# Optimization experiments

Hardware: AMD Instinct MI355X
Metric: run time of the kernel (lower is better)

The kernel has to match this reference:

```python
import jax, jax.numpy as jnp
import numpy as np

B, S, D = 2, 2048, 2048
H, Dh = 16, 128  # qkv_features = H*Dh = 2048
NEG = -1e10


def setup_inputs() -> dict:
    key = jax.random.key(0)
    k1, k2, k3 = jax.random.split(key, 3)
    x = jax.random.normal(k1, (B, S, D), dtype=jnp.float32)
    # variance_scaling(1.0, 'fan_in', 'normal') ~ std = 1/sqrt(fan_in)
    Wqkv = jax.random.normal(k2, (D, 3 * H * Dh), dtype=jnp.float32) / np.sqrt(D)
    bqkv = jnp.zeros((3 * H * Dh,), dtype=jnp.float32)
    Wout = jax.random.normal(k3, (H * Dh, D), dtype=jnp.float32) / np.sqrt(H * Dh)
    bout = jnp.zeros((D,), dtype=jnp.float32)
    return {"x": x, "Wqkv": Wqkv, "bqkv": bqkv, "Wout": Wout, "bout": bout}


def reference(x, Wqkv, bqkv, Wout, bout):
    b, s, _ = x.shape
    # fused QKV projection
    qkv = x @ Wqkv + bqkv                                   # [B, S, 3*H*Dh]
    qkv = qkv.reshape(b, s, 3, H, Dh).transpose(2, 0, 3, 1, 4)  # [3, B, H, S, Dh]
    q, k, v = qkv[0], qkv[1], qkv[2]
    scale = 1.0 / jnp.sqrt(jnp.asarray(Dh, dtype=x.dtype))
    # Each query chunk attends to the full key sequence with a causal mask,
    # which is mathematically full causal attention.
    scores = jnp.einsum('bhqd,bhkd->bhqk', q, k) * scale    # [B, H, S, S]
    causal = jnp.arange(s)[None, :] <= jnp.arange(s)[:, None]  # k <= q
    scores = jnp.where(causal[None, None, :, :], scores, NEG)
    weights = jax.nn.softmax(scores, axis=-1)
    out = jnp.einsum('bhqk,bhkd->bhqd', weights, v)         # [B, H, S, Dh]
    out = out.transpose(0, 2, 1, 3).reshape(b, s, H * Dh)
    return out @ Wout + bout
```

## Files before the change

### kernel.cpp

```cpp
#include <hip/hip_runtime.h>


typedef unsigned short u16;
typedef __attribute__((ext_vector_type(8))) short bf16x8;
typedef __attribute__((ext_vector_type(4))) float f32x4;

#define MFMA(a, b, c) __builtin_amdgcn_mfma_f32_16x16x32_bf16((a), (b), (c), 0, 0, 0)

__device__ __forceinline__ u16 f2bf(float f) {
    unsigned u = __builtin_bit_cast(unsigned, f);
    u += 0x7fffu + ((u >> 16) & 1u);
    return (u16)(u >> 16);
}

__device__ __forceinline__ void gload16(const void* g, void* l) {
    __builtin_amdgcn_global_load_lds(
        (const __attribute__((address_space(1))) void*)g,
        (__attribute__((address_space(3))) void*)l, 16, 0, 0);
}


__global__ __launch_bounds__(256) void k_cast(const float* __restrict__ src,
                                              u16* __restrict__ dst, int n4) {
    int i = blockIdx.x * 256 + threadIdx.x;
    if (i >= n4) return;
    float4 a = ((const float4*)src)[i];
    ushort4 r;
    r.x = f2bf(a.x); r.y = f2bf(a.y); r.z = f2bf(a.z); r.w = f2bf(a.w);
    ((ushort4*)dst)[i] = r;
}

__global__ __launch_bounds__(256) void k_castT(const float* __restrict__ src,
                                               u16* __restrict__ dst, int rows, int cols) {
    __shared__ float t[32][33];
    int c0 = blockIdx.x * 32, r0 = blockIdx.y * 32;
    int tx = threadIdx.x, ty = threadIdx.y;
#pragma unroll
    for (int i = 0; i < 4; ++i)
        t[ty + 8 * i][tx] = src[(size_t)(r0 + ty + 8 * i) * cols + (c0 + tx)];
    __syncthreads();
#pragma unroll
    for (int i = 0; i < 4; ++i)
        dst[(size_t)(c0 + ty + 8 * i) * rows + (r0 + tx)] = f2bf(t[tx][ty + 8 * i]);
}

__global__ __launch_bounds__(256) void k_transv(const u16* __restrict__ v,
                                                u16* __restrict__ vT) {
    __shared__ u16 t[32][33];
    int head = blockIdx.z;
    int s0 = blockIdx.x * 32, d0 = blockIdx.y * 32;
    const u16* vp = v + (size_t)head * 2048 * 128;
    u16* op = vT + (size_t)head * 128 * 2048;
    int tx = threadIdx.x, ty = threadIdx.y;
#pragma unroll
    for (int i = 0; i < 4; ++i)
        t[ty + 8 * i][tx] = vp[(size_t)(s0 + ty + 8 * i) * 128 + d0 + tx];
    __syncthreads();
#pragma unroll
    for (int i = 0; i < 4; ++i)
        op[(size_t)(d0 + 8 * i + ty) * 2048 + (s0 + tx)] = t[tx][ty + 8 * i];
}


template <int K>
__device__ __forceinline__ void gemm_core64(const u16* __restrict__ A,
                                            const u16* __restrict__ BT,
                                            int m0, int n0,
                                            f32x4 (&acc)[4][4],
                                            u16* As, u16* Bs) {
    const int tid = threadIdx.x, wave = tid >> 6, lane = tid & 63;
    const int wr = (wave >> 1) * 64, wc = (wave & 1) * 64;
    char* AsB = (char*)As;
    char* BsB = (char*)Bs;
    for (int k0 = 0; k0 < K; k0 += 64) {
        __syncthreads();
#pragma unroll
        for (int i = 0; i < 4; ++i) {
            int cb = (i * 4 + wave) * 64;
            int d = (cb + lane) * 16;
            int row = d >> 7;
            int co = (d & 127) ^ ((row & 7) << 4);
            gload16(A + (size_t)(m0 + row) * K + k0 + (co >> 1), AsB + cb * 16);
            gload16(BT + (size_t)(n0 + row) * K + k0 + (co >> 1), BsB + cb * 16);
        }
        __syncthreads();
        bf16x8 a[2][4], b[2][4];
#pragma unroll
        for (int ks = 0; ks < 2; ++ks)
#pragma unroll
            for (int m = 0; m < 4; ++m) {
                int row = wr + m * 16 + (lane & 15);
                a[ks][m] = *(const bf16x8*)(AsB +
                    ((row * 128 + ks * 64 + (lane >> 4) * 16) ^ ((row & 7) << 4)));
            }
#pragma unroll
        for (int ks = 0; ks < 2; ++ks)
#pragma unroll
            for (int n = 0; n < 4; ++n) {
                int row = wc + n * 16 + (lane & 15);
                b[ks][n] = *(const bf16x8*)(BsB +
                    ((row * 128 + ks * 64 + (lane >> 4) * 16) ^ ((row & 7) << 4)));
            }
        __builtin_amdgcn_s_setprio(1);
#pragma unroll
        for (int ks = 0; ks < 2; ++ks)
#pragma unroll
            for (int m = 0; m < 4; ++m)
#pragma unroll
                for (int n = 0; n < 4; ++n)
                    acc[m][n] = MFMA(a[ks][m], b[ks][n], acc[m][n]);
        __builtin_amdgcn_s_setprio(0);
    }
}

__global__ __launch_bounds__(256) void k_gemm_qkv(const u16* __restrict__ A,
                                                  const u16* __restrict__ BT,
                                                  const float* __restrict__ bias,
                                                  u16* __restrict__ q,
                                                  u16* __restrict__ kbuf,
                                                  u16* __restrict__ v) {
    __shared__ __align__(16) u16 As[128 * 64];
    __shared__ __align__(16) u16 Bs[128 * 64];
    f32x4 acc[4][4] = {};
    const int orig = blockIdx.y * 48 + blockIdx.x;
    const int xcd = orig & 7, idx = orig >> 3;
    const int n_blk = xcd * 6 + idx % 6, m_blk = idx / 6;
    const int m0 = m_blk * 128, n0 = n_blk * 128;
    gemm_core64<2048>(A, BT, m0, n0, acc, As, Bs);

    const int tid = threadIdx.x, wave = tid >> 6, lane = tid & 63;
    const int wr = (wave >> 1) * 64, wc = (wave & 1) * 64;
    const int t = n0 >> 11;
    u16* dst = (t == 0) ? q : (t == 1) ? kbuf : v;
#pragma unroll
    for (int m = 0; m < 4; ++m)
#pragma unroll
        for (int n = 0; n < 4; ++n)
#pragma unroll
            for (int j = 0; j < 4; ++j) {
                int gr = m0 + wr + m * 16 + (lane >> 4) * 4 + j;
                int gc = n0 + wc + n * 16 + (lane & 15);
                float val = acc[m][n][j] + bias[gc];
                int bb = gr >> 11, s = gr & 2047;
                int rem = gc & 2047, h = rem >> 7, d = rem & 127;
                dst[((size_t)(bb * 16 + h) * 2048 + s) * 128 + d] = f2bf(val);
            }
}

__global__ __launch_bounds__(256) void k_gemm_out(const u16* __restrict__ A,
                                                  const u16* __restrict__ BT,
                                                  const float* __restrict__ bias,
                                                  float* __restrict__ out) {
    __shared__ __align__(16) u16 As[128 * 64];
    __shared__ __align__(16) u16 Bs[128 * 64];
    f32x4 acc[4][4] = {};
    const int orig = blockIdx.y * 16 + blockIdx.x;
    const int nb = (orig & 7) * 64 + (orig >> 3);
    const int m0 = (nb / 16) * 128, n0 = (nb % 16) * 128;
    gemm_core64<2048>(A, BT, m0, n0, acc, As, Bs);

    const int tid = threadIdx.x, wave = tid >> 6, lane = tid & 63;
    const int wr = (wave >> 1) * 64, wc = (wave & 1) * 64;
#pragma unroll
    for (int m = 0; m < 4; ++m)
#pragma unroll
        for (int n = 0; n < 4; ++n)
#pragma unroll
            for (int j = 0; j < 4; ++j) {
                int gr = m0 + wr + m * 16 + (lane >> 4) * 4 + j;
                int gc = n0 + wc + n * 16 + (lane & 15);
                out[(size_t)gr * 2048 + gc] = acc[m][n][j] + bias[gc];
            }
}

__global__ __launch_bounds__(512) void k_attn(const u16* __restrict__ q,
                                              const u16* __restrict__ k,
                                              const u16* __restrict__ vT,
                                              u16* __restrict__ o) {
    __shared__ __align__(16) u16 KsA[2 * 64 * 128];
    __shared__ __align__(16) u16 VsA[2 * 128 * 64];
    __shared__ __align__(16) u16 PsA[8 * 16 * 64];
    char* ksB = (char*)KsA;
    char* vsB = (char*)VsA;

    const int tid = threadIdx.x, wave = tid >> 6, lane = tid & 63;
    char* psB = (char*)PsA + wave * 2048;

    const int lin = blockIdx.x;
    const int dd = (lin & 7) * 32 + (lin >> 3);
    const int head = dd >> 3, pair = dd & 7;

    const u16* qh = q + (size_t)head * 2048 * 128;
    const u16* kh = k + (size_t)head * 2048 * 128;
    const u16* vh = vT + (size_t)head * 128 * 2048;
    const int bb = head >> 4, hh = head & 15;
    const float qscale = 0.1275293562566334f;
    const float MFIX = 20.f;

    bf16x8 ones;
#pragma unroll
    for (int e = 0; e < 8; ++e) ones[e] = (short)0x3F80;

    auto stage = [&](int kv0, int bufsel) {
        char* kd = ksB + bufsel * 16384;
        char* vd = vsB + bufsel * 16384;
#pragma unroll
        for (int i = 0; i < 2; ++i) {
            int cb = (i * 8 + wave) * 64;
            int d = (cb + lane) * 16;
            int r = d >> 8;
            int co = (d & 255) ^ ((r & 7) << 4);
            gload16(kh + (size_t)(kv0 + r) * 128 + (co >> 1), kd + cb * 16);
        }
#pragma unroll
        for (int i = 0; i < 2; ++i) {
            int cb = (i * 8 + wave) * 64;
            int d = (cb + lane) * 16;
            int vr = d >> 7;
            int co = (d & 127) ^ ((vr & 7) << 4);
            gload16(vh + (size_t)vr * 2048 + kv0 + (co >> 1), vd + cb * 16);
        }
    };

#pragma unroll 1
    for (int qsel = 0; qsel < 2; ++qsel) {
        const int qi = qsel ? (15 - pair) : pair;
        const int q0 = qi * 128;
        const int ntile = 2 * qi + 2;

        bf16x8 qf[4];
        const int qr = q0 + wave * 16 + (lane & 15);
#pragma unroll
        for (int kt = 0; kt < 4; ++kt)
            qf[kt] = *(const bf16x8*)(qh + (size_t)qr * 128 + kt * 32 + (lane >> 4) * 8);

        f32x4 o_acc[8] = {};
        f32x4 l_r = {};

        stage(0, 0);
        int buf = 0;

#pragma unroll 1
        for (int t = 0; t < ntile; ++t) {
            const int kv0 = t * 64;
            if (t + 1 < ntile) {
                stage(kv0 + 64, buf ^ 1);
                asm volatile("s_waitcnt vmcnt(4)" ::: "memory");
            } else {
                asm volatile("s_waitcnt vmcnt(0)" ::: "memory");
            }
            __builtin_amdgcn_s_barrier();
            char* kb_ = ksB + buf * 16384;
            char* vb_ = vsB + buf * 16384;

            if (kv0 <= q0 + wave * 16 + 15) {
                f32x4 s_acc[4] = {};
                __builtin_amdgcn_s_setprio(1);
#pragma unroll
                for (int c = 0; c < 4; ++c) {
                    int row = c * 16 + (lane & 15);
#pragma unroll
                    for (int kt = 0; kt < 4; ++kt) {
                        bf16x8 kbf = *(const bf16x8*)(kb_ +
                            ((row * 256 + kt * 64 + (lane >> 4) * 16) ^ ((row & 7) << 4)));
                        s_acc[c] = MFMA(qf[kt], kbf, s_acc[c]);
                    }
                }
                __builtin_amdgcn_s_setprio(0);

                const bool maskblk = (kv0 + 64 > q0 + wave * 16);
#pragma unroll
                for (int j = 0; j < 4; ++j) {
                    int qg = q0 + wave * 16 + (lane >> 4) * 4 + j;
#pragma unroll
                    for (int c = 0; c < 4; ++c) {
                        float sv = fmaf(s_acc[c][j], qscale, -MFIX);
                        if (maskblk && (kv0 + c * 16 + (lane & 15)) > qg) sv = -1e30f;
                        s_acc[c][j] = exp2f(sv);
                    }
                }

#pragma unroll
                for (int c = 0; c < 4; ++c)
#pragma unroll
                    for (int j = 0; j < 4; ++j) {
                        int row = (lane >> 4) * 4 + j;
                        *(u16*)(psB + ((row * 128 + (c * 16 + (lane & 15)) * 2) ^ ((row & 7) << 4)))
                            = f2bf(s_acc[c][j]);
                    }
                bf16x8 pf[2];
#pragma unroll
                for (int kt = 0; kt < 2; ++kt) {
                    int row2 = lane & 15;
                    pf[kt] = *(const bf16x8*)(psB +
                        ((row2 * 128 + kt * 64 + (lane >> 4) * 16) ^ ((row2 & 7) << 4)));
                }

                __builtin_amdgcn_s_setprio(1);
                l_r = MFMA(pf[0], ones, l_r);
                l_r = MFMA(pf[1], ones, l_r);
#pragma unroll
                for (int c2 = 0; c2 < 8; ++c2) {
#pragma unroll
                    for (int kt = 0; kt < 2; ++kt) {
                        int row = c2 * 16 + (lane & 15);
                        bf16x8 vf = *(const bf16x8*)(vb_ +
                            ((row * 128 + kt * 64 + (lane >> 4) * 16) ^ ((row & 7) << 4)));
                        o_acc[c2] = MFMA(pf[kt], vf, o_acc[c2]);
                    }
                }
                __builtin_amdgcn_s_setprio(0);
            }

            __builtin_amdgcn_s_barrier();
            buf ^= 1;
        }

        float linv[4];
#pragma unroll
        for (int j = 0; j < 4; ++j) linv[j] = 1.0f / l_r[j];
#pragma unroll
        for (int c2 = 0; c2 < 8; ++c2)
#pragma unroll
            for (int j = 0; j < 4; ++j) {
                int qg = q0 + wave * 16 + (lane >> 4) * 4 + j;
                int d2 = c2 * 16 + (lane & 15);
                o[((size_t)(bb * 2048 + qg)) * 2048 + hh * 128 + d2]
                    = f2bf(o_acc[c2][j] * linv[j]);
            }
    }
}


extern "C" void kernel_launch(void* const* d_in, const int* in_sizes, int n_in,
                              void* d_out, int out_size, void* d_ws, size_t ws_size,
                              hipStream_t stream) {
    const float* x    = (const float*)d_in[0];
    const float* Wqkv = (const float*)d_in[1];
    const float* bqkv = (const float*)d_in[2];
    const float* Wout = (const float*)d_in[3];
    const float* bout = (const float*)d_in[4];
    float* out = (float*)d_out;

    char* ws = (char*)d_ws;
    const size_t SZ = 16777216;
    u16* q   = (u16*)(ws);
    u16* kb  = (u16*)(ws + SZ);
    u16* v   = (u16*)(ws + 2 * SZ);
    u16* vT  = (u16*)(ws + 3 * SZ);
    u16* ao  = v;
    u16* xb  = (u16*)(ws + 4 * SZ);
    u16* WqT = (u16*)(ws + 5 * SZ);
    u16* WoT = (u16*)(ws + 5 * SZ + 25165824);

    k_cast<<<dim3(8192), dim3(256), 0, stream>>>(x, xb, 2097152);
    k_castT<<<dim3(192, 64), dim3(32, 8), 0, stream>>>(Wqkv, WqT, 2048, 6144);
    k_castT<<<dim3(64, 64), dim3(32, 8), 0, stream>>>(Wout, WoT, 2048, 2048);
    k_gemm_qkv<<<dim3(48, 32), dim3(256), 0, stream>>>(xb, WqT, bqkv, q, kb, v);
    k_transv<<<dim3(64, 4, 32), dim3(32, 8), 0, stream>>>(v, vT);
    k_attn<<<dim3(256), dim3(512), 0, stream>>>(q, kb, vT, ao);
    k_gemm_out<<<dim3(16, 32), dim3(256), 0, stream>>>(ao, WoT, bout, out);
}
```

Baseline: 253.2 us.

## Split long causal query tiles across KV blocks and read V from global

The attention launch grows from 256 to 768 blocks. Each block handles one 128-row query tile and a range of KV tiles, driven by a packed lookup table. For the longer tiles (qi >= 8) the KV range is split in two; each half writes unnormalized fp32 partial outputs and row sums to workspace, and a new k_final kernel adds the halves, normalizes and writes bf16. V fragments are now read straight from global memory instead of being staged through LDS, which halves the async staging traffic and frees shared memory. The aim is better load balance and more parallelism across CUs. The cost is an extra kernel, extra fp32 traffic, and possibly less efficient uncoalesced global V reads.

```diff
diff --git a/kernel.cpp b/kernel.cpp
--- a/kernel.cpp
+++ b/kernel.cpp
@@ -2,6 +2,7 @@
 
 
 typedef unsigned short u16;
+typedef unsigned long long u64;
 typedef __attribute__((ext_vector_type(8))) short bf16x8;
 typedef __attribute__((ext_vector_type(4))) float f32x4;
 
@@ -176,19 +177,28 @@
 __global__ __launch_bounds__(512) void k_attn(const u16* __restrict__ q,
                                               const u16* __restrict__ k,
                                               const u16* __restrict__ vT,
-                                              u16* __restrict__ o) {
+                                              u16* __restrict__ o,
+                                              float* __restrict__ Opart,
+                                              float* __restrict__ Lpart) {
     __shared__ __align__(16) u16 KsA[2 * 64 * 128];
-    __shared__ __align__(16) u16 VsA[2 * 128 * 64];
     __shared__ __align__(16) u16 PsA[8 * 16 * 64];
     char* ksB = (char*)KsA;
-    char* vsB = (char*)VsA;
 
     const int tid = threadIdx.x, wave = tid >> 6, lane = tid & 63;
     char* psB = (char*)PsA + wave * 2048;
 
     const int lin = blockIdx.x;
-    const int dd = (lin & 7) * 32 + (lin >> 3);
-    const int head = dd >> 3, pair = dd & 7;
+    const int x = lin & 7, local = lin >> 3;
+    const int head = x * 4 + (local & 3);
+    const int e = local >> 2;
+    const u64 qiT0 = 0x9AA5BBCC6DDEE7FFull;
+    const u64 qiT1 = 0x0000000001238849ull;
+    const u64 ptT  = 0x0000AA4912449124ull;
+    const int qi   = (int)(((e < 16 ? (qiT0 >> (e * 4)) : (qiT1 >> ((e - 16) * 4)))) & 15);
+    const int part = (int)((ptT >> (2 * e)) & 3);
+    const int q0 = qi * 128;
+    const int t0 = (part == 1) ? (qi + 1) : 0;
+    const int t1 = (part == 0) ? (qi + 1) : (2 * qi + 2);
 
     const u16* qh = q + (size_t)head * 2048 * 128;
     const u16* kh = k + (size_t)head * 2048 * 128;
@@ -199,11 +209,10 @@
 
     bf16x8 ones;
 #pragma unroll
-    for (int e = 0; e < 8; ++e) ones[e] = (short)0x3F80;
-
-    auto stage = [&](int kv0, int bufsel) {
+    for (int ee = 0; ee < 8; ++ee) ones[ee] = (short)0x3F80;
+
+    auto stageK = [&](int kv0, int bufsel) {
         char* kd = ksB + bufsel * 16384;
-        char* vd = vsB + bufsel * 16384;
 #pragma unroll
         for (int i = 0; i < 2; ++i) {
             int cb = (i * 8 + wave) * 64;
@@ -212,110 +221,96 @@
             int co = (d & 255) ^ ((r & 7) << 4);
             gload16(kh + (size_t)(kv0 + r) * 128 + (co >> 1), kd + cb * 16);
         }
-#pragma unroll
-        for (int i = 0; i < 2; ++i) {
-            int cb = (i * 8 + wave) * 64;
-            int d = (cb + lane) * 16;
-            int vr = d >> 7;
-            int co = (d & 127) ^ ((vr & 7) << 4);
-            gload16(vh + (size_t)vr * 2048 + kv0 + (co >> 1), vd + cb * 16);
+    };
+
+    bf16x8 qf[4];
+    const int qr = q0 + wave * 16 + (lane & 15);
+#pragma unroll
+    for (int kt = 0; kt < 4; ++kt)
+        qf[kt] = *(const bf16x8*)(qh + (size_t)qr * 128 + kt * 32 + (lane >> 4) * 8);
+
+    f32x4 o_acc[8] = {};
+    f32x4 l_r = {};
+
+    stageK(t0 * 64, 0);
+    int buf = 0;
+
+#pragma unroll 1
+    for (int t = t0; t < t1; ++t) {
+        const int kv0 = t * 64;
+        if (t + 1 < t1) {
+            stageK(kv0 + 64, buf ^ 1);
+            asm volatile("s_waitcnt vmcnt(2)" ::: "memory");
+        } else {
+            asm volatile("s_waitcnt vmcnt(0)" ::: "memory");
         }
-    };
-
-#pragma unroll 1
-    for (int qsel = 0; qsel < 2; ++qsel) {
-        const int qi = qsel ? (15 - pair) : pair;
-        const int q0 = qi * 128;
-        const int ntile = 2 * qi + 2;
-
-        bf16x8 qf[4];
-        const int qr = q0 + wave * 16 + (lane & 15);
-#pragma unroll
-        for (int kt = 0; kt < 4; ++kt)
-            qf[kt] = *(const bf16x8*)(qh + (size_t)qr * 128 + kt * 32 + (lane >> 4) * 8);
-
-        f32x4 o_acc[8] = {};
-        f32x4 l_r = {};
-
-        stage(0, 0);
-        int buf = 0;
-
-#pragma unroll 1
-        for (int t = 0; t < ntile; ++t) {
-            const int kv0 = t * 64;
-            if (t + 1 < ntile) {
-                stage(kv0 + 64, buf ^ 1);
-                asm volatile("s_waitcnt vmcnt(4)" ::: "memory");
-            } else {
-                asm volatile("s_waitcnt vmcnt(0)" ::: "memory");
-            }
-            __builtin_amdgcn_s_barrier();
-            char* kb_ = ksB + buf * 16384;
-            char* vb_ = vsB + buf * 16384;
-
-            if (kv0 <= q0 + wave * 16 + 15) {
-                f32x4 s_acc[4] = {};
-                __builtin_amdgcn_s_setprio(1);
+        __builtin_amdgcn_s_barrier();
+        char* kb_ = ksB + buf * 16384;
+
+        if (kv0 <= q0 + wave * 16 + 15) {
+            f32x4 s_acc[4] = {};
+            __builtin_amdgcn_s_setprio(1);
+#pragma unroll
+            for (int c = 0; c < 4; ++c) {
+                int row = c * 16 + (lane & 15);
+#pragma unroll
+                for (int kt = 0; kt < 4; ++kt) {
+                    bf16x8 kbf = *(const bf16x8*)(kb_ +
+                        ((row * 256 + kt * 64 + (lane >> 4) * 16) ^ ((row & 7) << 4)));
+                    s_acc[c] = MFMA(qf[kt], kbf, s_acc[c]);
+                }
+            }
+            __builtin_amdgcn_s_setprio(0);
+
+            const bool maskblk = (kv0 + 64 > q0 + wave * 16);
+#pragma unroll
+            for (int j = 0; j < 4; ++j) {
+                int qg = q0 + wave * 16 + (lane >> 4) * 4 + j;
 #pragma unroll
                 for (int c = 0; c < 4; ++c) {
-                    int row = c * 16 + (lane & 15);
-#pragma unroll
-                    for (int kt = 0; kt < 4; ++kt) {
-                        bf16x8 kbf = *(const bf16x8*)(kb_ +
-                            ((row * 256 + kt * 64 + (lane >> 4) * 16) ^ ((row & 7) << 4)));
-                        s_acc[c] = MFMA(qf[kt], kbf, s_acc[c]);
-                    }
+                    float sv = fmaf(s_acc[c][j], qscale, -MFIX);
+                    if (maskblk && (kv0 + c * 16 + (lane & 15)) > qg) sv = -1e30f;
+                    s_acc[c][j] = exp2f(sv);
                 }
-                __builtin_amdgcn_s_setprio(0);
-
-                const bool maskblk = (kv0 + 64 > q0 + wave * 16);
+            }
+
+#pragma unroll
+            for (int c = 0; c < 4; ++c)
 #pragma unroll
                 for (int j = 0; j < 4; ++j) {
-                    int qg = q0 + wave * 16 + (lane >> 4) * 4 + j;
-#pragma unroll
-                    for (int c = 0; c < 4; ++c) {
-                        float sv = fmaf(s_acc[c][j], qscale, -MFIX);
-                        if (maskblk && (kv0 + c * 16 + (lane & 15)) > qg) sv = -1e30f;
-                        s_acc[c][j] = exp2f(sv);
-                    }
+                    int row = (lane >> 4) * 4 + j;
+                    *(u16*)(psB + ((row * 128 + (c * 16 + (lane & 15)) * 2) ^ ((row & 7) << 4)))
+                        = f2bf(s_acc[c][j]);
                 }
-
-#pragma unroll
-                for (int c = 0; c < 4; ++c)
-#pragma unroll
-                    for (int j = 0; j < 4; ++j) {
-                        int row = (lane >> 4) * 4 + j;
-                        *(u16*)(psB + ((row * 128 + (c * 16 + (lane & 15)) * 2) ^ ((row & 7) << 4)))
-                            = f2bf(s_acc[c][j]);
-                    }
-                bf16x8 pf[2];
+            bf16x8 pf[2];
+#pragma unroll
+            for (int kt = 0; kt < 2; ++kt) {
+                int row2 = lane & 15;
+                pf[kt] = *(const bf16x8*)(psB +
+                    ((row2 * 128 + kt * 64 + (lane >> 4) * 16) ^ ((row2 & 7) << 4)));
+            }
+
+            __builtin_amdgcn_s_setprio(1);
+            l_r = MFMA(pf[0], ones, l_r);
+            l_r = MFMA(pf[1], ones, l_r);
+#pragma unroll
+            for (int c2 = 0; c2 < 8; ++c2) {
+                int row = c2 * 16 + (lane & 15);
 #pragma unroll
                 for (int kt = 0; kt < 2; ++kt) {
-                    int row2 = lane & 15;
-                    pf[kt] = *(const bf16x8*)(psB +
-                        ((row2 * 128 + kt * 64 + (lane >> 4) * 16) ^ ((row2 & 7) << 4)));
+                    bf16x8 vf = *(const bf16x8*)(vh + (size_t)row * 2048 + kv0 +
+                                                 kt * 32 + (lane >> 4) * 8);
+                    o_acc[c2] = MFMA(pf[kt], vf, o_acc[c2]);
                 }
-
-                __builtin_amdgcn_s_setprio(1);
-                l_r = MFMA(pf[0], ones, l_r);
-                l_r = MFMA(pf[1], ones, l_r);
-#pragma unroll
-                for (int c2 = 0; c2 < 8; ++c2) {
-#pragma unroll
-                    for (int kt = 0; kt < 2; ++kt) {
-                        int row = c2 * 16 + (lane & 15);
-                        bf16x8 vf = *(const bf16x8*)(vb_ +
-                            ((row * 128 + kt * 64 + (lane >> 4) * 16) ^ ((row & 7) << 4)));
-                        o_acc[c2] = MFMA(pf[kt], vf, o_acc[c2]);
-                    }
-                }
-                __builtin_amdgcn_s_setprio(0);
-            }
-
-            __builtin_amdgcn_s_barrier();
-            buf ^= 1;
+            }
+            __builtin_amdgcn_s_setprio(0);
         }
 
+        __builtin_amdgcn_s_barrier();
+        buf ^= 1;
+    }
+
+    if (part == 2) {
         float linv[4];
 #pragma unroll
         for (int j = 0; j < 4; ++j) linv[j] = 1.0f / l_r[j];
@@ -328,6 +323,48 @@
                 o[((size_t)(bb * 2048 + qg)) * 2048 + hh * 128 + d2]
                     = f2bf(o_acc[c2][j] * linv[j]);
             }
+    } else {
+        const int qe = qi - 8;
+        float* Op = Opart + (((size_t)(part * 32 + head) * 8 + qe) * 128) * 128;
+#pragma unroll
+        for (int c2 = 0; c2 < 8; ++c2)
+#pragma unroll
+            for (int j = 0; j < 4; ++j) {
+                int row = wave * 16 + (lane >> 4) * 4 + j;
+                int d2 = c2 * 16 + (lane & 15);
+                Op[row * 128 + d2] = o_acc[c2][j];
+            }
+        if ((lane & 15) == 0) {
+#pragma unroll
+            for (int j = 0; j < 4; ++j) {
+                int row = wave * 16 + (lane >> 4) * 4 + j;
+                Lpart[(size_t)part * 32 * 8 * 128 + ((head * 8 + qe) * 128 + row)] = l_r[j];
+            }
+        }
+    }
+}
+
+__global__ __launch_bounds__(256) void k_final(const float* __restrict__ Opart,
+                                               const float* __restrict__ Lpart,
+                                               u16* __restrict__ o) {
+    const int head = blockIdx.x >> 3, qe = blockIdx.x & 7;
+    const int row = threadIdx.x >> 1, dh = (threadIdx.x & 1) * 64;
+    const size_t tileoff = (((size_t)head * 8 + qe) * 128 + row) * 128 + dh;
+    const float* p0 = Opart + tileoff;
+    const float* p1 = p0 + (size_t)32 * 8 * 128 * 128;
+    const float l = Lpart[(head * 8 + qe) * 128 + row] +
+                    Lpart[32 * 8 * 128 + (head * 8 + qe) * 128 + row];
+    const float linv = 1.0f / l;
+    const int s = (qe + 8) * 128 + row, bb = head >> 4, hh = head & 15;
+    u16* dst = o + ((size_t)(bb * 2048 + s)) * 2048 + hh * 128 + dh;
+#pragma unroll
+    for (int i = 0; i < 16; ++i) {
+        float4 a = ((const float4*)p0)[i];
+        float4 b = ((const float4*)p1)[i];
+        ushort4 r;
+        r.x = f2bf((a.x + b.x) * linv); r.y = f2bf((a.y + b.y) * linv);
+        r.z = f2bf((a.z + b.z) * linv); r.w = f2bf((a.w + b.w) * linv);
+        ((ushort4*)dst)[i] = r;
     }
 }
 
@@ -352,12 +389,15 @@
     u16* xb  = (u16*)(ws + 4 * SZ);
     u16* WqT = (u16*)(ws + 5 * SZ);
     u16* WoT = (u16*)(ws + 5 * SZ + 25165824);
+    float* Opart = (float*)(ws + 4 * SZ);
+    float* Lpart = (float*)(ws + 4 * SZ + 33554432);
 
     k_cast<<<dim3(8192), dim3(256), 0, stream>>>(x, xb, 2097152);
     k_castT<<<dim3(192, 64), dim3(32, 8), 0, stream>>>(Wqkv, WqT, 2048, 6144);
     k_castT<<<dim3(64, 64), dim3(32, 8), 0, stream>>>(Wout, WoT, 2048, 2048);
     k_gemm_qkv<<<dim3(48, 32), dim3(256), 0, stream>>>(xb, WqT, bqkv, q, kb, v);
     k_transv<<<dim3(64, 4, 32), dim3(32, 8), 0, stream>>>(v, vT);
-    k_attn<<<dim3(256), dim3(512), 0, stream>>>(q, kb, vT, ao);
+    k_attn<<<dim3(768), dim3(512), 0, stream>>>(q, kb, vT, ao, Opart, Lpart);
+    k_final<<<dim3(256), dim3(256), 0, stream>>>(Opart, Lpart, ao);
     k_gemm_out<<<dim3(16, 32), dim3(256), 0, stream>>>(ao, WoT, bout, out);
 }
```

Measured after the change: 394.9 us. 1.56x slower.
